# Kernel optimization log

Hardware: AMD Instinct MI355X
Metric: run time of the kernel (lower is better)

## Reference

```python
import jax, jax.numpy as jnp
import numpy as np

N = 300000   # nodes
E = 1500000  # edges
G = 30000    # graphs
R = 3        # relations
EMB = 32
HID = 64
OUT = 2


def rgcn_conv(x, src, dst, edge_type, W, root, bias, num_nodes):
    """PyG RGCNConv: out_i = x_i @ root + bias + sum_r mean_{j in N_r(i)} x_j @ W_r."""
    out = x @ root + bias
    for r in range(W.shape[0]):
        xr = x @ W[r]                                  # [N, out] transform once per relation
        mask = (edge_type == r).astype(x.dtype)        # [E]
        msg = xr[src] * mask[:, None]                  # gather + mask  [E, out]
        agg = jax.ops.segment_sum(msg, dst, num_segments=num_nodes)
        cnt = jax.ops.segment_sum(mask, dst, num_segments=num_nodes)
        out = out + agg / jnp.maximum(cnt, 1.0)[:, None]
    return out


def global_mean_pool(x, batch, num_graphs):
    s = jax.ops.segment_sum(x, batch, num_segments=num_graphs)
    c = jax.ops.segment_sum(jnp.ones((x.shape[0],), x.dtype), batch, num_segments=num_graphs)
    return s / jnp.maximum(c, 1.0)[:, None]


def setup_inputs() -> dict:
    key = jax.random.key(0)
    ks = jax.random.split(key, 16)
    def glorot(k, shape):
        fan_in, fan_out = shape[-2], shape[-1]
        lim = np.sqrt(6.0 / (fan_in + fan_out)).astype(np.float32)
        return jax.random.uniform(k, shape, jnp.float32, -lim, lim)
    return {
        "sid": jax.random.randint(ks[0], (N,), 0, 26),
        "cid": jax.random.randint(ks[1], (N,), 0, 10),
        "pid": jax.random.randint(ks[2], (N,), 0, 128),
        "edge_index": jax.random.randint(ks[3], (2, E), 0, N),
        "edge_type": jax.random.randint(ks[4], (E,), 0, R),
        "batch": jnp.sort(jax.random.randint(ks[5], (N,), 0, G)),
        "num_graphs": G,
        "shape_emb": jax.random.normal(ks[6], (26, EMB), jnp.float32),
        "col_emb": jax.random.normal(ks[7], (10, EMB), jnp.float32),
        "pos_emb": jax.random.normal(ks[8], (128, EMB), jnp.float32),
        "W1": glorot(ks[9], (R, EMB, HID)),
        "root1": glorot(ks[10], (EMB, HID)),
        "b1": jnp.zeros((HID,), jnp.float32),
        "W2": glorot(ks[11], (R, HID, HID)),
        "root2": glorot(ks[12], (HID, HID)),
        "b2": jnp.zeros((HID,), jnp.float32),
        "lin_W": glorot(ks[13], (HID, OUT)),
        "lin_b": jnp.zeros((OUT,), jnp.float32),
    }


def reference(sid, cid, pid, edge_index, edge_type, batch, num_graphs,
              shape_emb, col_emb, pos_emb,
              W1, root1, b1, W2, root2, b2, lin_W, lin_b):
    num_nodes = sid.shape[0]
    src, dst = edge_index[0], edge_index[1]
    x = shape_emb[sid] + col_emb[cid] + pos_emb[pid]          # [N, 32]
    x = jax.nn.relu(rgcn_conv(x, src, dst, edge_type, W1, root1, b1, num_nodes))
    x = jax.nn.relu(rgcn_conv(x, src, dst, edge_type, W2, root2, b2, num_nodes))
    g = global_mean_pool(x, batch, num_graphs)                 # [G, 64]
    return g @ lin_W + lin_b                                   # [G, 2]
```

## Files before the change

### kernel.cpp

```cpp
#include <hip/hip_runtime.h>
#include <hip/hip_bf16.h>

#define NREL 3
#define EMB 32
#define HID 64
#define OVCAP 1024
#define BCAP 1024

typedef __attribute__((ext_vector_type(8))) short short8_t;
typedef __attribute__((ext_vector_type(4))) short short4_t;
typedef __attribute__((ext_vector_type(4))) float f32x4;

__device__ inline short f2bf(float v) {
  __hip_bfloat16 b = __float2bfloat16(v);
  short s;
  __builtin_memcpy(&s, &b, 2);
  return s;
}
__device__ inline float bf2f(short s) {
  __hip_bfloat16 b;
  __builtin_memcpy(&b, &s, 2);
  return __bfloat162float(b);
}
__device__ inline void split8(const float* v, short8_t* h, short8_t* l) {
#pragma unroll
  for (int i = 0; i < 8; i++) {
    short hh = f2bf(v[i]);
    (*h)[i] = hh;
    (*l)[i] = f2bf(v[i] - bf2f(hh));
  }
}

__global__ __launch_bounds__(256) void prep_k(
    const int* __restrict__ sid, const int* __restrict__ cid, const int* __restrict__ pid,
    const float* __restrict__ se, const float* __restrict__ ce, const float* __restrict__ pe,
    short* __restrict__ xh, short* __restrict__ xl,
    const int* __restrict__ src, const int* __restrict__ dst, const int* __restrict__ et,
    int* __restrict__ bcur, unsigned* __restrict__ pk,
    const float* __restrict__ root1, const float* __restrict__ W1,
    const float* __restrict__ root2, const float* __restrict__ W2,
    short* __restrict__ w1h, short* __restrict__ w1l,
    short* __restrict__ w2h, short* __restrict__ w2l, int N, int E) {
  int i = blockIdx.x * 256 + threadIdx.x;
  if (i < N * 8) {
    int n = i >> 3, cg = i & 7;
    const float4 a = *(const float4*)&se[sid[n] * EMB + cg * 4];
    const float4 b = *(const float4*)&ce[cid[n] * EMB + cg * 4];
    const float4 c = *(const float4*)&pe[pid[n] * EMB + cg * 4];
    float v[4];
    v[0] = a.x + b.x + c.x; v[1] = a.y + b.y + c.y;
    v[2] = a.z + b.z + c.z; v[3] = a.w + b.w + c.w;
    short4_t h, l;
#pragma unroll
    for (int j = 0; j < 4; j++) {
      short hh = f2bf(v[j]);
      h[j] = hh;
      l[j] = f2bf(v[j] - bf2f(hh));
    }
    *(short4_t*)&xh[(size_t)n * EMB + cg * 4] = h;
    *(short4_t*)&xl[(size_t)n * EMB + cg * 4] = l;
  }
  if (i < E) {
    int d = dst[i];
    int b = d >> 6;
    int j = atomicAdd(&bcur[b * 16], 1);
    if (j < BCAP)
      pk[(size_t)b * BCAP + j] =
          ((unsigned)(d & 63) << 21) | ((unsigned)et[i] << 19) | (unsigned)src[i];
  }
  if (i < 64 * 128) {
    int k = i >> 6, n = i & 63;
    float v = (k < EMB) ? root1[k * 64 + n] : W1[(k - EMB) * 64 + n];
    short h = f2bf(v);
    w1h[n * 128 + k] = h;
    w1l[n * 128 + k] = f2bf(v - bf2f(h));
  }
  if (i < 64 * 256) {
    int k = i >> 6, n = i & 63;
    float v = (k < HID) ? root2[k * 64 + n] : W2[(k - HID) * 64 + n];
    short h = f2bf(v);
    w2h[n * 256 + k] = h;
    w2l[n * 256 + k] = f2bf(v - bf2f(h));
  }
}

__global__ __launch_bounds__(256) void l1fused_k(
    const short* __restrict__ xh, const short* __restrict__ xl,
    const int* __restrict__ bcur, const unsigned* __restrict__ pk,
    const short* __restrict__ wth, const short* __restrict__ wtl,
    const float* __restrict__ bias, short* __restrict__ h1h, short* __restrict__ h1l, int N) {
  __shared__ __align__(16) short lws[64][16][8];
  __shared__ __align__(16) short gh_s[192][4][8];
  __shared__ __align__(16) short gl_s[192][4][8];
  __shared__ __align__(16) int4 mid_s[192];
  __shared__ int cnt_s[192];
  __shared__ unsigned ovf_s[OVCAP];
  __shared__ int ovfn_s;

  const int t = threadIdx.x;
  const int lane = t & 63, w = t >> 6;
  const int m_ = lane & 15, q = lane >> 4;
  const int n0b = blockIdx.x * 64;

  int node_c = n0b + w * 16 + m_;
  if (node_c >= N) node_c = N - 1;
  short8_t ah0 = *(const short8_t*)&xh[(size_t)node_c * EMB + q * 8];
  short8_t al0 = *(const short8_t*)&xl[(size_t)node_c * EMB + q * 8];
#pragma unroll
  for (int i = 0; i < 4; i++) {
    int chi = t + 256 * i;
    int row = chi >> 4, c = chi & 15;
    short8_t wv = *(const short8_t*)&wth[(size_t)row * 128 + c * 8];
    *(short8_t*)&lws[row][c ^ (row & 7)][0] = wv;
  }
  if (t < 192) cnt_s[t] = 0;
  if (t == 0) ovfn_s = 0;
  __syncthreads();

  {
    int ne = bcur[blockIdx.x * 16];
    if (ne > BCAP) ne = BCAP;
    const size_t base = (size_t)blockIdx.x * BCAP;
    for (int e = t; e < ne; e += 256) {
      unsigned p = pk[base + e];
      int srcn = (int)(p & 0x7FFFF);
      int slot = (int)((p >> 19) & 3) * 64 + (int)(p >> 21);
      int j = atomicAdd(&cnt_s[slot], 1);
      if (j < 4) ((int*)&mid_s[slot])[j] = srcn;
      else {
        int k2 = atomicAdd(&ovfn_s, 1);
        if (k2 < OVCAP) ovf_s[k2] = ((unsigned)slot << 19) | (unsigned)srcn;
      }
    }
  }
  __syncthreads();

  {
    int ovn = ovfn_s;
    if (ovn > OVCAP) ovn = OVCAP;
    int tslot[3], tq[3], tlen[3];
    int4 tid4[3];
#pragma unroll
    for (int k = 0; k < 3; k++) {
      int tau = t + 256 * k;
      tslot[k] = tau >> 2;
      tq[k] = tau & 3;
      tid4[k] = mid_s[tslot[k]];
      tlen[k] = cnt_s[tslot[k]];
    }
    short8_t v0[3], v1[3], v2[3], v3[3];
#pragma unroll
    for (int k = 0; k < 3; k++) {
      int nself = n0b + (tslot[k] & 63);
      if (nself >= N) nself = N - 1;
      int g0 = (0 < tlen[k]) ? tid4[k].x : nself;
      int g1 = (1 < tlen[k]) ? tid4[k].y : nself;
      int g2 = (2 < tlen[k]) ? tid4[k].z : nself;
      int g3 = (3 < tlen[k]) ? tid4[k].w : nself;
      size_t co = (size_t)tq[k] * 8;
      v0[k] = *(const short8_t*)&xh[(size_t)g0 * EMB + co];
      v1[k] = *(const short8_t*)&xh[(size_t)g1 * EMB + co];
      v2[k] = *(const short8_t*)&xh[(size_t)g2 * EMB + co];
      v3[k] = *(const short8_t*)&xh[(size_t)g3 * EMB + co];
    }
#pragma unroll
    for (int k = 0; k < 3; k++) {
      float a[8];
      float k0 = (0 < tlen[k]) ? 1.f : 0.f;
      float k1 = (1 < tlen[k]) ? 1.f : 0.f;
      float k2 = (2 < tlen[k]) ? 1.f : 0.f;
      float k3 = (3 < tlen[k]) ? 1.f : 0.f;
#pragma unroll
      for (int i = 0; i < 8; i++)
        a[i] = k0 * bf2f(v0[k][i]) + k1 * bf2f(v1[k][i]) + k2 * bf2f(v2[k][i]) +
               k3 * bf2f(v3[k][i]);
      for (int k3_ = 0; k3_ < ovn; k3_++) {
        unsigned ov = ovf_s[k3_];
        if ((int)(ov >> 19) == tslot[k]) {
          short8_t u = *(const short8_t*)&xh[(size_t)(ov & 0x7FFFF) * EMB + tq[k] * 8];
#pragma unroll
          for (int i = 0; i < 8; i++) a[i] += bf2f(u[i]);
        }
      }
      float inv = 1.f / fmaxf((float)tlen[k], 1.f);
#pragma unroll
      for (int i = 0; i < 8; i++) a[i] *= inv;
      short8_t hi, lo;
      split8(a, &hi, &lo);
      int qs = tq[k] ^ (tslot[k] & 3);
      *(short8_t*)&gh_s[tslot[k]][qs][0] = hi;
      *(short8_t*)&gl_s[tslot[k]][qs][0] = lo;
    }
  }
  __syncthreads();

  f32x4 acc[4];
#pragma unroll
  for (int i = 0; i < 4; i++) acc[i] = (f32x4){0.f, 0.f, 0.f, 0.f};
  short8_t ahv[4], alv[4];
#pragma unroll
  for (int g = 0; g < 4; g++) {
    if (g == 0) {
      ahv[0] = ah0;
      alv[0] = al0;
    } else {
      int slot = (g - 1) * 64 + w * 16 + m_;
      int qs = q ^ (slot & 3);
      ahv[g] = *(const short8_t*)&gh_s[slot][qs][0];
      alv[g] = *(const short8_t*)&gl_s[slot][qs][0];
    }
#pragma unroll
    for (int tt = 0; tt < 4; tt++) {
      int row = 16 * tt + m_;
      int cs = (g * 4 + q) ^ (row & 7);
      short8_t bh = *(const short8_t*)&lws[row][cs][0];
      acc[tt] = __builtin_amdgcn_mfma_f32_16x16x32_bf16(ahv[g], bh, acc[tt], 0, 0, 0);
      acc[tt] = __builtin_amdgcn_mfma_f32_16x16x32_bf16(alv[g], bh, acc[tt], 0, 0, 0);
    }
  }
  __syncthreads();

#pragma unroll
  for (int i = 0; i < 4; i++) {
    int chi = t + 256 * i;
    int row = chi >> 4, c = chi & 15;
    short8_t wv = *(const short8_t*)&wtl[(size_t)row * 128 + c * 8];
    *(short8_t*)&lws[row][c ^ (row & 7)][0] = wv;
  }
  __syncthreads();

#pragma unroll
  for (int g = 0; g < 4; g++) {
#pragma unroll
    for (int tt = 0; tt < 4; tt++) {
      int row = 16 * tt + m_;
      int cs = (g * 4 + q) ^ (row & 7);
      short8_t bl = *(const short8_t*)&lws[row][cs][0];
      acc[tt] = __builtin_amdgcn_mfma_f32_16x16x32_bf16(ahv[g], bl, acc[tt], 0, 0, 0);
    }
  }
#pragma unroll
  for (int tt = 0; tt < 4; tt++) {
    float bia = bias[16 * tt + m_];
#pragma unroll
    for (int reg = 0; reg < 4; reg++) {
      int node = n0b + w * 16 + q * 4 + reg;
      if (node < N) {
        float val = fmaxf(acc[tt][reg] + bia, 0.f);
        short hh = f2bf(val);
        h1h[(size_t)node * HID + 16 * tt + m_] = hh;
        h1l[(size_t)node * HID + 16 * tt + m_] = f2bf(val - bf2f(hh));
      }
    }
  }
}

__global__ __launch_bounds__(256) void l2fused_k(
    const short* __restrict__ h1h, const short* __restrict__ h1l,
    const int* __restrict__ bcur, const unsigned* __restrict__ pk,
    const short* __restrict__ wth, const short* __restrict__ wtl,
    const float* __restrict__ bias, const float* __restrict__ linW,
    const int* __restrict__ batch, float* __restrict__ gs, float* __restrict__ gc, int N) {
  __shared__ __align__(16) short lws[64][16][8];
  __shared__ __align__(16) short gh_s[192][4][8];
  __shared__ __align__(16) short gl_s[192][4][8];
  __shared__ __align__(16) int4 mid_s[192];
  __shared__ int cnt_s[192];
  __shared__ unsigned ovf_s[OVCAP];
  __shared__ int ovfn_s;

  const int t = threadIdx.x;
  const int lane = t & 63, w = t >> 6;
  const int m_ = lane & 15, q = lane >> 4;
  const int n0b = blockIdx.x * 64;

  int node_c = n0b + w * 16 + m_;
  if (node_c >= N) node_c = N - 1;
  short8_t ash[2], asl[2];
#pragma unroll
  for (int s_ = 0; s_ < 2; s_++) {
    ash[s_] = *(const short8_t*)&h1h[(size_t)node_c * HID + s_ * 32 + q * 8];
    asl[s_] = *(const short8_t*)&h1l[(size_t)node_c * HID + s_ * 32 + q * 8];
  }
#pragma unroll
  for (int i = 0; i < 4; i++) {
    int chi = t + 256 * i;
    int row = chi >> 4, c = chi & 15;
    int g = c >> 2, qq = c & 3;
    short8_t wv = *(const short8_t*)&wth[(size_t)row * 256 + g * 64 + 0 * 32 + qq * 8];
    *(short8_t*)&lws[row][c ^ (row & 7)][0] = wv;
  }
  if (t < 192) cnt_s[t] = 0;
  if (t == 0) ovfn_s = 0;
  __syncthreads();

  {
    int ne = bcur[blockIdx.x * 16];
    if (ne > BCAP) ne = BCAP;
    const size_t base = (size_t)blockIdx.x * BCAP;
    for (int e = t; e < ne; e += 256) {
      unsigned p = pk[base + e];
      int srcn = (int)(p & 0x7FFFF);
      int slot = (int)((p >> 19) & 3) * 64 + (int)(p >> 21);
      int j = atomicAdd(&cnt_s[slot], 1);
      if (j < 4) ((int*)&mid_s[slot])[j] = srcn;
      else {
        int k2 = atomicAdd(&ovfn_s, 1);
        if (k2 < OVCAP) ovf_s[k2] = ((unsigned)slot << 19) | (unsigned)srcn;
      }
    }
  }
  __syncthreads();

  f32x4 acc[4];
#pragma unroll
  for (int i = 0; i < 4; i++) acc[i] = (f32x4){0.f, 0.f, 0.f, 0.f};

  int ovn = ovfn_s;
  if (ovn > OVCAP) ovn = OVCAP;

#pragma unroll
  for (int s_ = 0; s_ < 2; s_++) {
    if (s_ == 1) {
#pragma unroll
      for (int i = 0; i < 4; i++) {
        int chi = t + 256 * i;
        int row = chi >> 4, c = chi & 15;
        int g = c >> 2, q2 = c & 3;
        short8_t wv = *(const short8_t*)&wth[(size_t)row * 256 + g * 64 + 32 + q2 * 8];
        *(short8_t*)&lws[row][c ^ (row & 7)][0] = wv;
      }
    }
    int tslot[3], tq[3], tlen[3];
    int4 tid4[3];
#pragma unroll
    for (int k = 0; k < 3; k++) {
      int tau = t + 256 * k;
      tslot[k] = tau >> 2;
      tq[k] = tau & 3;
      tid4[k] = mid_s[tslot[k]];
      tlen[k] = cnt_s[tslot[k]];
    }
    short8_t v0[3], v1[3], v2[3], v3[3];
#pragma unroll
    for (int k = 0; k < 3; k++) {
      int nself = n0b + (tslot[k] & 63);
      if (nself >= N) nself = N - 1;
      int g0 = (0 < tlen[k]) ? tid4[k].x : nself;
      int g1 = (1 < tlen[k]) ? tid4[k].y : nself;
      int g2 = (2 < tlen[k]) ? tid4[k].z : nself;
      int g3 = (3 < tlen[k]) ? tid4[k].w : nself;
      size_t co = (size_t)s_ * 32 + tq[k] * 8;
      v0[k] = *(const short8_t*)&h1h[(size_t)g0 * HID + co];
      v1[k] = *(const short8_t*)&h1h[(size_t)g1 * HID + co];
      v2[k] = *(const short8_t*)&h1h[(size_t)g2 * HID + co];
      v3[k] = *(const short8_t*)&h1h[(size_t)g3 * HID + co];
    }
#pragma unroll
    for (int k = 0; k < 3; k++) {
      float a[8];
      float k0 = (0 < tlen[k]) ? 1.f : 0.f;
      float k1 = (1 < tlen[k]) ? 1.f : 0.f;
      float k2 = (2 < tlen[k]) ? 1.f : 0.f;
      float k3 = (3 < tlen[k]) ? 1.f : 0.f;
#pragma unroll
      for (int i = 0; i < 8; i++)
        a[i] = k0 * bf2f(v0[k][i]) + k1 * bf2f(v1[k][i]) + k2 * bf2f(v2[k][i]) +
               k3 * bf2f(v3[k][i]);
      for (int k3_ = 0; k3_ < ovn; k3_++) {
        unsigned ov = ovf_s[k3_];
        if ((int)(ov >> 19) == tslot[k]) {
          short8_t u = *(const short8_t*)&h1h[(size_t)(ov & 0x7FFFF) * HID + s_ * 32 +
                                              tq[k] * 8];
#pragma unroll
          for (int i = 0; i < 8; i++) a[i] += bf2f(u[i]);
        }
      }
      float inv = 1.f / fmaxf((float)tlen[k], 1.f);
#pragma unroll
      for (int i = 0; i < 8; i++) a[i] *= inv;
      short8_t hi, lo;
      split8(a, &hi, &lo);
      int qs = tq[k] ^ (tslot[k] & 3);
      *(short8_t*)&gh_s[tslot[k]][qs][0] = hi;
      *(short8_t*)&gl_s[tslot[k]][qs][0] = lo;
    }
    __syncthreads();

    short8_t ahv[4], alv[4];
#pragma unroll
    for (int g = 0; g < 4; g++) {
      if (g == 0) {
        ahv[0] = ash[s_];
        alv[0] = asl[s_];
      } else {
        int slot = (g - 1) * 64 + w * 16 + m_;
        int qs = q ^ (slot & 3);
        ahv[g] = *(const short8_t*)&gh_s[slot][qs][0];
        alv[g] = *(const short8_t*)&gl_s[slot][qs][0];
      }
#pragma unroll
      for (int tt = 0; tt < 4; tt++) {
        int row = 16 * tt + m_;
        int cs = (g * 4 + q) ^ (row & 7);
        short8_t bh = *(const short8_t*)&lws[row][cs][0];
        acc[tt] = __builtin_amdgcn_mfma_f32_16x16x32_bf16(ahv[g], bh, acc[tt], 0, 0, 0);
        acc[tt] = __builtin_amdgcn_mfma_f32_16x16x32_bf16(alv[g], bh, acc[tt], 0, 0, 0);
      }
    }
    __syncthreads();

#pragma unroll
    for (int i = 0; i < 4; i++) {
      int chi = t + 256 * i;
      int row = chi >> 4, c = chi & 15;
      int g = c >> 2, q2 = c & 3;
      short8_t wv = *(const short8_t*)&wtl[(size_t)row * 256 + g * 64 + s_ * 32 + q2 * 8];
      *(short8_t*)&lws[row][c ^ (row & 7)][0] = wv;
    }
    __syncthreads();

#pragma unroll
    for (int g = 0; g < 4; g++) {
#pragma unroll
      for (int tt = 0; tt < 4; tt++) {
        int row = 16 * tt + m_;
        int cs = (g * 4 + q) ^ (row & 7);
        short8_t bl = *(const short8_t*)&lws[row][cs][0];
        acc[tt] = __builtin_amdgcn_mfma_f32_16x16x32_bf16(ahv[g], bl, acc[tt], 0, 0, 0);
      }
    }
    if (s_ == 0) __syncthreads();
  }

  float bia[4], lw0[4], lw1[4];
#pragma unroll
  for (int tt = 0; tt < 4; tt++) {
    int col = 16 * tt + m_;
    bia[tt] = bias[col];
    lw0[tt] = linW[col * 2 + 0];
    lw1[tt] = linW[col * 2 + 1];
  }
#pragma unroll
  for (int reg = 0; reg < 4; reg++) {
    int node = n0b + w * 16 + q * 4 + reg;
    float p0 = 0.f, p1 = 0.f;
#pragma unroll
    for (int tt = 0; tt < 4; tt++) {
      float v = fmaxf(acc[tt][reg] + bia[tt], 0.f);
      p0 += v * lw0[tt];
      p1 += v * lw1[tt];
    }
#pragma unroll
    for (int o = 1; o < 16; o <<= 1) {
      p0 += __shfl_xor(p0, o, 64);
      p1 += __shfl_xor(p1, o, 64);
    }
    if (m_ == 0 && node < N) {
      int g = batch[node];
      atomicAdd(&gs[g * 2 + 0], p0);
      atomicAdd(&gs[g * 2 + 1], p1);
      atomicAdd(&gc[g], 1.0f);
    }
  }
}

__global__ __launch_bounds__(256) void final_k(const float* __restrict__ gs,
                                               const float* __restrict__ gc,
                                               const float* __restrict__ linb,
                                               float* __restrict__ out, int G) {
  int i = blockIdx.x * 256 + threadIdx.x;
  if (i >= G * 2) return;
  int g = i >> 1, o = i & 1;
  out[i] = gs[i] / fmaxf(gc[g], 1.0f) + linb[o];
}

extern "C" void kernel_launch(void* const* d_in, const int* in_sizes, int n_in,
                              void* d_out, int out_size, void* d_ws, size_t ws_size,
                              hipStream_t stream) {
  const int* sid = (const int*)d_in[0];
  const int* cid = (const int*)d_in[1];
  const int* pid = (const int*)d_in[2];
  const int* ei = (const int*)d_in[3];
  const int* et = (const int*)d_in[4];
  const int* batch = (const int*)d_in[5];
  const float* se = (const float*)d_in[7];
  const float* ce = (const float*)d_in[8];
  const float* pe = (const float*)d_in[9];
  const float* W1 = (const float*)d_in[10];
  const float* root1 = (const float*)d_in[11];
  const float* b1 = (const float*)d_in[12];
  const float* W2 = (const float*)d_in[13];
  const float* root2 = (const float*)d_in[14];
  const float* b2 = (const float*)d_in[15];
  const float* linW = (const float*)d_in[16];
  const float* linb = (const float*)d_in[17];
  float* out = (float*)d_out;

  const int N = in_sizes[0];
  const int E = in_sizes[4];
  const int G = out_size / 2;
  const int* src = ei;
  const int* dst = ei + E;
  const int NBk = (N + 63) / 64;
  const int NBa = (NBk + 15) & ~15;

  char* w = (char*)d_ws;
  short* h1h = (short*)w;  w += (size_t)N * HID * sizeof(short);
  short* h1l = (short*)w;  w += (size_t)N * HID * sizeof(short);
  short* xh = (short*)w;   w += (size_t)N * EMB * sizeof(short);
  short* xl = (short*)w;   w += (size_t)N * EMB * sizeof(short);
  float* gs = (float*)w;   w += (size_t)G * 2 * sizeof(float);
  float* gc = (float*)w;   w += (size_t)G * sizeof(float);
  int* bcur = (int*)w;     w += (size_t)NBa * 16 * sizeof(int);
  unsigned* pk = (unsigned*)w; w += (size_t)NBa * BCAP * sizeof(unsigned);
  short* w1h = (short*)w;  w += (size_t)64 * 128 * sizeof(short);
  short* w1l = (short*)w;  w += (size_t)64 * 128 * sizeof(short);
  short* w2h = (short*)w;  w += (size_t)64 * 256 * sizeof(short);
  short* w2l = (short*)w;  w += (size_t)64 * 256 * sizeof(short);
  if ((size_t)(w - (char*)d_ws) > ws_size) return;

  hipMemsetAsync(bcur, 0, (size_t)NBa * 16 * sizeof(int), stream);
  hipMemsetAsync(gs, 0, (size_t)G * 3 * sizeof(float), stream);

  int prep_n = N * 8;
  if (prep_n < E) prep_n = E;
  if (prep_n < 64 * 256) prep_n = 64 * 256;
  prep_k<<<(prep_n + 255) / 256, 256, 0, stream>>>(sid, cid, pid, se, ce, pe, xh, xl, src,
                                                   dst, et, bcur, pk, root1, W1, root2, W2,
                                                   w1h, w1l, w2h, w2l, N, E);

  l1fused_k<<<NBk, 256, 0, stream>>>(xh, xl, bcur, pk, w1h, w1l, b1, h1h, h1l, N);
  l2fused_k<<<NBk, 256, 0, stream>>>(h1h, h1l, bcur, pk, w2h, w2l, b2, linW, batch, gs, gc,
                                     N);
  final_k<<<(G * 2 + 255) / 256, 256, 0, stream>>>(gs, gc, linb, out, G);
}
```

Baseline: 387.0 us.

## Gather neighbor means directly into MFMA operand registers, dropping LDS staging

Each lane now gathers and averages neighbor features for exactly the rows and k-slices it later feeds as MFMA A operands. The hi/lo split results go straight into registers instead of round-tripping through the gh_s/gl_s shared buffers. This removes a shared-memory write/read pass and a block barrier in both layer kernels and cuts LDS footprint, which may raise occupancy. In layer 2, both 32-column halves are gathered up front, which raises register pressure.

Result: no change. 379.6 us (-1.9%).

```diff
diff --git a/kernel.cpp b/kernel.cpp
--- a/kernel.cpp
+++ b/kernel.cpp
@@ -90,8 +90,6 @@
     const short* __restrict__ wth, const short* __restrict__ wtl,
     const float* __restrict__ bias, short* __restrict__ h1h, short* __restrict__ h1l, int N) {
   __shared__ __align__(16) short lws[64][16][8];
-  __shared__ __align__(16) short gh_s[192][4][8];
-  __shared__ __align__(16) short gl_s[192][4][8];
   __shared__ __align__(16) int4 mid_s[192];
   __shared__ int cnt_s[192];
   __shared__ unsigned ovf_s[OVCAP];
@@ -135,16 +133,17 @@
   }
   __syncthreads();
 
+  short8_t ahv[4], alv[4];
+  ahv[0] = ah0;
+  alv[0] = al0;
   {
     int ovn = ovfn_s;
     if (ovn > OVCAP) ovn = OVCAP;
-    int tslot[3], tq[3], tlen[3];
+    int tslot[3], tlen[3];
     int4 tid4[3];
 #pragma unroll
     for (int k = 0; k < 3; k++) {
-      int tau = t + 256 * k;
-      tslot[k] = tau >> 2;
-      tq[k] = tau & 3;
+      tslot[k] = k * 64 + w * 16 + m_;
       tid4[k] = mid_s[tslot[k]];
       tlen[k] = cnt_s[tslot[k]];
     }
@@ -157,7 +156,7 @@
       int g1 = (1 < tlen[k]) ? tid4[k].y : nself;
       int g2 = (2 < tlen[k]) ? tid4[k].z : nself;
       int g3 = (3 < tlen[k]) ? tid4[k].w : nself;
-      size_t co = (size_t)tq[k] * 8;
+      size_t co = (size_t)q * 8;
       v0[k] = *(const short8_t*)&xh[(size_t)g0 * EMB + co];
       v1[k] = *(const short8_t*)&xh[(size_t)g1 * EMB + co];
       v2[k] = *(const short8_t*)&xh[(size_t)g2 * EMB + co];
@@ -177,7 +176,7 @@
       for (int k3_ = 0; k3_ < ovn; k3_++) {
         unsigned ov = ovf_s[k3_];
         if ((int)(ov >> 19) == tslot[k]) {
-          short8_t u = *(const short8_t*)&xh[(size_t)(ov & 0x7FFFF) * EMB + tq[k] * 8];
+          short8_t u = *(const short8_t*)&xh[(size_t)(ov & 0x7FFFF) * EMB + q * 8];
 #pragma unroll
           for (int i = 0; i < 8; i++) a[i] += bf2f(u[i]);
         }
@@ -185,30 +184,15 @@
       float inv = 1.f / fmaxf((float)tlen[k], 1.f);
 #pragma unroll
       for (int i = 0; i < 8; i++) a[i] *= inv;
-      short8_t hi, lo;
-      split8(a, &hi, &lo);
-      int qs = tq[k] ^ (tslot[k] & 3);
-      *(short8_t*)&gh_s[tslot[k]][qs][0] = hi;
-      *(short8_t*)&gl_s[tslot[k]][qs][0] = lo;
-    }
-  }
-  __syncthreads();
+      split8(a, &ahv[k + 1], &alv[k + 1]);
+    }
+  }
 
   f32x4 acc[4];
 #pragma unroll
   for (int i = 0; i < 4; i++) acc[i] = (f32x4){0.f, 0.f, 0.f, 0.f};
-  short8_t ahv[4], alv[4];
 #pragma unroll
   for (int g = 0; g < 4; g++) {
-    if (g == 0) {
-      ahv[0] = ah0;
-      alv[0] = al0;
-    } else {
-      int slot = (g - 1) * 64 + w * 16 + m_;
-      int qs = q ^ (slot & 3);
-      ahv[g] = *(const short8_t*)&gh_s[slot][qs][0];
-      alv[g] = *(const short8_t*)&gl_s[slot][qs][0];
-    }
 #pragma unroll
     for (int tt = 0; tt < 4; tt++) {
       int row = 16 * tt + m_;
@@ -262,8 +246,6 @@
     const float* __restrict__ bias, const float* __restrict__ linW,
     const int* __restrict__ batch, float* __restrict__ gs, float* __restrict__ gc, int N) {
   __shared__ __align__(16) short lws[64][16][8];
-  __shared__ __align__(16) short gh_s[192][4][8];
-  __shared__ __align__(16) short gl_s[192][4][8];
   __shared__ __align__(16) int4 mid_s[192];
   __shared__ int cnt_s[192];
   __shared__ unsigned ovf_s[OVCAP];
@@ -276,12 +258,6 @@
 
   int node_c = n0b + w * 16 + m_;
   if (node_c >= N) node_c = N - 1;
-  short8_t ash[2], asl[2];
-#pragma unroll
-  for (int s_ = 0; s_ < 2; s_++) {
-    ash[s_] = *(const short8_t*)&h1h[(size_t)node_c * HID + s_ * 32 + q * 8];
-    asl[s_] = *(const short8_t*)&h1l[(size_t)node_c * HID + s_ * 32 + q * 8];
-  }
 #pragma unroll
   for (int i = 0; i < 4; i++) {
     int chi = t + 256 * i;
@@ -312,13 +288,103 @@
   }
   __syncthreads();
 
+  short8_t ahv0[4], alv0[4], ahv1[4], alv1[4];
+  {
+    ahv0[0] = *(const short8_t*)&h1h[(size_t)node_c * HID + q * 8];
+    alv0[0] = *(const short8_t*)&h1l[(size_t)node_c * HID + q * 8];
+    ahv1[0] = *(const short8_t*)&h1h[(size_t)node_c * HID + 32 + q * 8];
+    alv1[0] = *(const short8_t*)&h1l[(size_t)node_c * HID + 32 + q * 8];
+    int ovn = ovfn_s;
+    if (ovn > OVCAP) ovn = OVCAP;
+    int tslot[3], tlen[3];
+    int4 tid4[3];
+    int gid[3][4];
+#pragma unroll
+    for (int k = 0; k < 3; k++) {
+      tslot[k] = k * 64 + w * 16 + m_;
+      tid4[k] = mid_s[tslot[k]];
+      tlen[k] = cnt_s[tslot[k]];
+      int nself = n0b + (tslot[k] & 63);
+      if (nself >= N) nself = N - 1;
+      gid[k][0] = (0 < tlen[k]) ? tid4[k].x : nself;
+      gid[k][1] = (1 < tlen[k]) ? tid4[k].y : nself;
+      gid[k][2] = (2 < tlen[k]) ? tid4[k].z : nself;
+      gid[k][3] = (3 < tlen[k]) ? tid4[k].w : nself;
+    }
+    float a0[3][8], a1[3][8];
+    {
+      short8_t v0[3], v1[3], v2[3], v3[3];
+#pragma unroll
+      for (int k = 0; k < 3; k++) {
+        size_t co = (size_t)q * 8;
+        v0[k] = *(const short8_t*)&h1h[(size_t)gid[k][0] * HID + co];
+        v1[k] = *(const short8_t*)&h1h[(size_t)gid[k][1] * HID + co];
+        v2[k] = *(const short8_t*)&h1h[(size_t)gid[k][2] * HID + co];
+        v3[k] = *(const short8_t*)&h1h[(size_t)gid[k][3] * HID + co];
+      }
+#pragma unroll
+      for (int k = 0; k < 3; k++) {
+        float k0 = (0 < tlen[k]) ? 1.f : 0.f;
+        float k1 = (1 < tlen[k]) ? 1.f : 0.f;
+        float k2 = (2 < tlen[k]) ? 1.f : 0.f;
+        float k3 = (3 < tlen[k]) ? 1.f : 0.f;
+#pragma unroll
+        for (int i = 0; i < 8; i++)
+          a0[k][i] = k0 * bf2f(v0[k][i]) + k1 * bf2f(v1[k][i]) + k2 * bf2f(v2[k][i]) +
+                     k3 * bf2f(v3[k][i]);
+      }
+    }
+    {
+      short8_t v0[3], v1[3], v2[3], v3[3];
+#pragma unroll
+      for (int k = 0; k < 3; k++) {
+        size_t co = 32 + (size_t)q * 8;
+        v0[k] = *(const short8_t*)&h1h[(size_t)gid[k][0] * HID + co];
+        v1[k] = *(const short8_t*)&h1h[(size_t)gid[k][1] * HID + co];
+        v2[k] = *(const short8_t*)&h1h[(size_t)gid[k][2] * HID + co];
+        v3[k] = *(const short8_t*)&h1h[(size_t)gid[k][3] * HID + co];
+      }
+#pragma unroll
+      for (int k = 0; k < 3; k++) {
+        float k0 = (0 < tlen[k]) ? 1.f : 0.f;
+        float k1 = (1 < tlen[k]) ? 1.f : 0.f;
+        float k2 = (2 < tlen[k]) ? 1.f : 0.f;
+        float k3 = (3 < tlen[k]) ? 1.f : 0.f;
+#pragma unroll
+        for (int i = 0; i < 8; i++)
+          a1[k][i] = k0 * bf2f(v0[k][i]) + k1 * bf2f(v1[k][i]) + k2 * bf2f(v2[k][i]) +
+                     k3 * bf2f(v3[k][i]);
+      }
+    }
+#pragma unroll
+    for (int k = 0; k < 3; k++) {
+      for (int k3_ = 0; k3_ < ovn; k3_++) {
+        unsigned ov = ovf_s[k3_];
+        if ((int)(ov >> 19) == tslot[k]) {
+          const short* p = &h1h[(size_t)(ov & 0x7FFFF) * HID];
+          short8_t u0 = *(const short8_t*)&p[q * 8];
+          short8_t u1 = *(const short8_t*)&p[32 + q * 8];
+#pragma unroll
+          for (int i = 0; i < 8; i++) {
+            a0[k][i] += bf2f(u0[i]);
+            a1[k][i] += bf2f(u1[i]);
+          }
+        }
+      }
+      float inv = 1.f / fmaxf((float)tlen[k], 1.f);
+#pragma unroll
+      for (int i = 0; i < 8; i++) {
+        a0[k][i] *= inv;
+        a1[k][i] *= inv;
+      }
+      split8(a0[k], &ahv0[k + 1], &alv0[k + 1]);
+      split8(a1[k], &ahv1[k + 1], &alv1[k + 1]);
+    }
+  }
+
   f32x4 acc[4];
 #pragma unroll
   for (int i = 0; i < 4; i++) acc[i] = (f32x4){0.f, 0.f, 0.f, 0.f};
-
-  int ovn = ovfn_s;
-  if (ovn > OVCAP) ovn = OVCAP;
-
 #pragma unroll
   for (int s_ = 0; s_ < 2; s_++) {
     if (s_ == 1) {
@@ -330,86 +396,22 @@
         short8_t wv = *(const short8_t*)&wth[(size_t)row * 256 + g * 64 + 32 + q2 * 8];
         *(short8_t*)&lws[row][c ^ (row & 7)][0] = wv;
       }
-    }
-    int tslot[3], tq[3], tlen[3];
-    int4 tid4[3];
-#pragma unroll
-    for (int k = 0; k < 3; k++) {
-      int tau = t + 256 * k;
-      tslot[k] = tau >> 2;
-      tq[k] = tau & 3;
-      tid4[k] = mid_s[tslot[k]];
-      tlen[k] = cnt_s[tslot[k]];
-    }
-    short8_t v0[3], v1[3], v2[3], v3[3];
-#pragma unroll
-    for (int k = 0; k < 3; k++) {
-      int nself = n0b + (tslot[k] & 63);
-      if (nself >= N) nself = N - 1;
-      int g0 = (0 < tlen[k]) ? tid4[k].x : nself;
-      int g1 = (1 < tlen[k]) ? tid4[k].y : nself;
-      int g2 = (2 < tlen[k]) ? tid4[k].z : nself;
-      int g3 = (3 < tlen[k]) ? tid4[k].w : nself;
-      size_t co = (size_t)s_ * 32 + tq[k] * 8;
-      v0[k] = *(const short8_t*)&h1h[(size_t)g0 * HID + co];
-      v1[k] = *(const short8_t*)&h1h[(size_t)g1 * HID + co];
-      v2[k] = *(const short8_t*)&h1h[(size_t)g2 * HID + co];
-      v3[k] = *(const short8_t*)&h1h[(size_t)g3 * HID + co];
-    }
-#pragma unroll
-    for (int k = 0; k < 3; k++) {
-      float a[8];
-      float k0 = (0 < tlen[k]) ? 1.f : 0.f;
-      float k1 = (1 < tlen[k]) ? 1.f : 0.f;
-      float k2 = (2 < tlen[k]) ? 1.f : 0.f;
-      float k3 = (3 < tlen[k]) ? 1.f : 0.f;
-#pragma unroll
-      for (int i = 0; i < 8; i++)
-        a[i] = k0 * bf2f(v0[k][i]) + k1 * bf2f(v1[k][i]) + k2 * bf2f(v2[k][i]) +
-               k3 * bf2f(v3[k][i]);
-      for (int k3_ = 0; k3_ < ovn; k3_++) {
-        unsigned ov = ovf_s[k3_];
-        if ((int)(ov >> 19) == tslot[k]) {
-          short8_t u = *(const short8_t*)&h1h[(size_t)(ov & 0x7FFFF) * HID + s_ * 32 +
-                                              tq[k] * 8];
-#pragma unroll
-          for (int i = 0; i < 8; i++) a[i] += bf2f(u[i]);
-        }
-      }
-      float inv = 1.f / fmaxf((float)tlen[k], 1.f);
-#pragma unroll
-      for (int i = 0; i < 8; i++) a[i] *= inv;
-      short8_t hi, lo;
-      split8(a, &hi, &lo);
-      int qs = tq[k] ^ (tslot[k] & 3);
-      *(short8_t*)&gh_s[tslot[k]][qs][0] = hi;
-      *(short8_t*)&gl_s[tslot[k]][qs][0] = lo;
-    }
-    __syncthreads();
-
-    short8_t ahv[4], alv[4];
+      __syncthreads();
+    }
 #pragma unroll
     for (int g = 0; g < 4; g++) {
-      if (g == 0) {
-        ahv[0] = ash[s_];
-        alv[0] = asl[s_];
-      } else {
-        int slot = (g - 1) * 64 + w * 16 + m_;
-        int qs = q ^ (slot & 3);
-        ahv[g] = *(const short8_t*)&gh_s[slot][qs][0];
-        alv[g] = *(const short8_t*)&gl_s[slot][qs][0];
-      }
+      short8_t ah = (s_ == 0) ? ahv0[g] : ahv1[g];
+      short8_t al = (s_ == 0) ? alv0[g] : alv1[g];
 #pragma unroll
       for (int tt = 0; tt < 4; tt++) {
         int row = 16 * tt + m_;
         int cs = (g * 4 + q) ^ (row & 7);
         short8_t bh = *(const short8_t*)&lws[row][cs][0];
-        acc[tt] = __builtin_amdgcn_mfma_f32_16x16x32_bf16(ahv[g], bh, acc[tt], 0, 0, 0);
-        acc[tt] = __builtin_amdgcn_mfma_f32_16x16x32_bf16(alv[g], bh, acc[tt], 0, 0, 0);
+        acc[tt] = __builtin_amdgcn_mfma_f32_16x16x32_bf16(ah, bh, acc[tt], 0, 0, 0);
+        acc[tt] = __builtin_amdgcn_mfma_f32_16x16x32_bf16(al, bh, acc[tt], 0, 0, 0);
       }
     }
     __syncthreads();
-
 #pragma unroll
     for (int i = 0; i < 4; i++) {
       int chi = t + 256 * i;
@@ -419,15 +421,15 @@
       *(short8_t*)&lws[row][c ^ (row & 7)][0] = wv;
     }
     __syncthreads();
-
 #pragma unroll
     for (int g = 0; g < 4; g++) {
+      short8_t ah = (s_ == 0) ? ahv0[g] : ahv1[g];
 #pragma unroll
       for (int tt = 0; tt < 4; tt++) {
         int row = 16 * tt + m_;
         int cs = (g * 4 + q) ^ (row & 7);
         short8_t bl = *(const short8_t*)&lws[row][cs][0];
-        acc[tt] = __builtin_amdgcn_mfma_f32_16x16x32_bf16(ahv[g], bl, acc[tt], 0, 0, 0);
+        acc[tt] = __builtin_amdgcn_mfma_f32_16x16x32_bf16(ah, bl, acc[tt], 0, 0, 0);
       }
     }
     if (s_ == 0) __syncthreads();
```
